# Kernel tuning notes

Hardware: AMD Instinct MI355X
Metric: run time of the kernel (lower is better)

The kernel has to match this reference:

```python
import jax, jax.numpy as jnp
import numpy as np

NEG = -1e9  # safe stand-in for log(0) in the one-hot initial state distribution


def setup_inputs() -> dict:
    key = jax.random.key(0)
    k1, k2 = jax.random.split(key)
    Q, S = 128, 96
    B, T = 2048, 48
    # log-space transition weights A[q, s, q']
    A = jax.random.normal(k1, (Q, S, Q), dtype=jnp.float32)
    # batch of symbol sequences
    xs = jax.random.randint(k2, (B, T), 0, S, dtype=jnp.int64)
    return {"A": A, "xs": xs}


def reference(A, xs):
    """FSA phonotactics log-likelihood: HMM-style forward algorithm in the log semiring.

    A:  [Q, S, Q] log-space weights (normalized per source state so that
        sum over (S, Q') of exp(A[q]) == 1, as in A_and_final_normalized).
    xs: [B, T] int symbol ids.
    Returns per-sequence log-likelihood [B] (final weights are all-ones).
    """
    Q, S, _ = A.shape
    B, T = xs.shape
    # normalize: each source state's outgoing mass sums to 1 in exp-space
    logZ = jax.nn.logsumexp(A.reshape(Q, -1), axis=-1)      # [Q]
    A_norm = A - logZ[:, None, None]                         # [Q, S, Q]
    # init = one-hot on state 0 (log-space)
    log_alpha0 = jnp.full((B, Q), NEG, dtype=A.dtype).at[:, 0].set(0.0)

    def step(log_alpha, tok):
        # tok: [B]; gather per-symbol transition matrices: [Q, B, Q]
        M = A_norm[:, tok, :]
        # alpha'[b, q'] = logsumexp_q( alpha[b, q] + M[q, b, q'] )
        la = jax.nn.logsumexp(log_alpha.T[:, :, None] + M, axis=0)  # [B, Q]
        return la, None

    log_alpha, _ = jax.lax.scan(step, log_alpha0, xs.T)  # scan over time
    # final = all ones -> vv(alpha, final) = sum over states (logsumexp in log space)
    return jax.nn.logsumexp(log_alpha, axis=-1)  # [B]
```

## Files before the change

kernel.cpp:

```cpp
#include <hip/hip_runtime.h>

#define QN 128
#define SN 96
#define TN 48
#define ROWSTRIDE (SN * QN)
#define NSEG 6
#define SEGLEN (ROWSTRIDE / NSEG)
#define SHIFT 10.0f
#define LOG255 5.5412635451584258f

#define U8_BYTES ((size_t)SN * QN * QN)
#define PART_OFF (U8_BYTES)
#define RMAX_OFF (PART_OFF + (size_t)QN * NSEG * 4)
#define LSC_OFF  (RMAX_OFF + (size_t)QN * NSEG * 4)
#define WS_NEED  (LSC_OFF + 16)

__global__ __launch_bounds__(256)
void fsa_stats(const float* __restrict__ A, float* __restrict__ part,
               float* __restrict__ rowmax) {
    const int bid = blockIdx.x;
    const int q   = bid / NSEG;
    const int seg = bid % NSEG;
    const int tid = threadIdx.x;
    const float* base = A + (size_t)q * ROWSTRIDE + seg * SEGLEN + tid * 8;

    const float4 v0 = *reinterpret_cast<const float4*>(base);
    const float4 v1 = *reinterpret_cast<const float4*>(base + 4);
    float s = (__expf(v0.x - SHIFT) + __expf(v0.y - SHIFT)) +
              (__expf(v0.z - SHIFT) + __expf(v0.w - SHIFT)) +
              (__expf(v1.x - SHIFT) + __expf(v1.y - SHIFT)) +
              (__expf(v1.z - SHIFT) + __expf(v1.w - SHIFT));
    float m = fmaxf(fmaxf(fmaxf(v0.x, v0.y), fmaxf(v0.z, v0.w)),
                    fmaxf(fmaxf(v1.x, v1.y), fmaxf(v1.z, v1.w)));

    __shared__ float reds[256];
    __shared__ float redm[256];
    reds[tid] = s; redm[tid] = m;
    __syncthreads();
    #pragma unroll
    for (int o = 128; o > 0; o >>= 1) {
        if (tid < o) {
            reds[tid] += reds[tid + o];
            redm[tid] = fmaxf(redm[tid], redm[tid + o]);
        }
        __syncthreads();
    }
    if (tid == 0) { part[bid] = reds[0]; rowmax[bid] = redm[0]; }
}

__global__ __launch_bounds__(256)
void fsa_write_u8(const float* __restrict__ A, const float* __restrict__ part,
                  const float* __restrict__ rowmax, uint* __restrict__ U,
                  float* __restrict__ logsc_p) {
    const int bid = blockIdx.x;
    const int kq  = bid / NSEG;
    const int seg = bid % NSEG;
    const int tid = threadIdx.x;

    __shared__ float lz[QN];
    __shared__ float dl[QN];
    if (tid < QN) {
        float z = 0.0f, rm = -1e30f;
        #pragma unroll
        for (int j = 0; j < NSEG; ++j) {
            z  += part[tid * NSEG + j];
            rm  = fmaxf(rm, rowmax[tid * NSEG + j]);
        }
        const float l = SHIFT + __logf(z);
        lz[tid] = l;
        dl[tid] = rm - l;
    }
    __syncthreads();
    #pragma unroll
    for (int o = 64; o > 0; o >>= 1) {
        if (tid < o) dl[tid] = fmaxf(dl[tid], dl[tid + o]);
        __syncthreads();
    }
    const float glob = dl[0];
    if (bid == 0 && tid == 0) logsc_p[0] = glob - LOG255;

    const int li = seg * SEGLEN + tid * 8;
    const int s  = li >> 7;
    const int qp = li & 127;

    uint d0 = 0, d1 = 0, d2 = 0, d3 = 0, d4 = 0, d5 = 0, d6 = 0, d7 = 0;
    #pragma unroll
    for (int j = 0; j < 4; ++j) {
        const int k = 4 * kq + j;
        const float* src = A + (size_t)k * ROWSTRIDE + li;
        const float off = lz[k] + glob;
        const float4 v0 = *reinterpret_cast<const float4*>(src);
        const float4 v1 = *reinterpret_cast<const float4*>(src + 4);
        const int sh = 8 * j;
        d0 |= ((uint)(255.0f * __expf(v0.x - off) + 0.5f)) << sh;
        d1 |= ((uint)(255.0f * __expf(v0.y - off) + 0.5f)) << sh;
        d2 |= ((uint)(255.0f * __expf(v0.z - off) + 0.5f)) << sh;
        d3 |= ((uint)(255.0f * __expf(v0.w - off) + 0.5f)) << sh;
        d4 |= ((uint)(255.0f * __expf(v1.x - off) + 0.5f)) << sh;
        d5 |= ((uint)(255.0f * __expf(v1.y - off) + 0.5f)) << sh;
        d6 |= ((uint)(255.0f * __expf(v1.z - off) + 0.5f)) << sh;
        d7 |= ((uint)(255.0f * __expf(v1.w - off) + 0.5f)) << sh;
    }
    uint* dst = U + (size_t)s * (QN * QN / 4) + kq * QN + qp;
    *reinterpret_cast<uint4*>(dst)     = make_uint4(d0, d1, d2, d3);
    *reinterpret_cast<uint4*>(dst + 4) = make_uint4(d4, d5, d6, d7);
}

__global__ __launch_bounds__(256)
void fsa_forward_u8(const uint* __restrict__ U, const int* __restrict__ xs,
                    const float* __restrict__ logsc_p, float* __restrict__ out,
                    int B) {
    const int wv   = threadIdx.x >> 6;
    const int lane = threadIdx.x & 63;
    const int b    = blockIdx.x * 4 + wv;
    if (b >= B) return;

    __shared__ __align__(16) float sp[4][QN];
    __shared__ int stok[4][TN];

    if (lane < TN) stok[wv][lane] = xs[b * TN + lane];
    sp[wv][2 * lane]     = (lane == 0) ? 1.0f : 0.0f;
    sp[wv][2 * lane + 1] = 0.0f;
    const float logsc = logsc_p[0];
    float c = 0.0f;

    for (int t = 0; t < TN; ++t) {
        int tok = __builtin_amdgcn_readfirstlane(stok[wv][t]);
        tok = (tok < 0) ? 0 : ((tok >= SN) ? (SN - 1) : tok);
        const uint2* wp = reinterpret_cast<const uint2*>(
            U + (size_t)tok * (QN * QN / 4)) + lane;

        float a0 = 0.0f, a1 = 0.0f;
        #pragma unroll 8
        for (int kq = 0; kq < 32; ++kq) {
            const uint2 w   = wp[kq * 64];
            const float4 pv = *reinterpret_cast<const float4*>(&sp[wv][4 * kq]);
            a0 = fmaf(pv.x, (float)( w.x        & 0xffu), a0);
            a0 = fmaf(pv.y, (float)((w.x >>  8) & 0xffu), a0);
            a0 = fmaf(pv.z, (float)((w.x >> 16) & 0xffu), a0);
            a0 = fmaf(pv.w, (float)( w.x >> 24         ), a0);
            a1 = fmaf(pv.x, (float)( w.y        & 0xffu), a1);
            a1 = fmaf(pv.y, (float)((w.y >>  8) & 0xffu), a1);
            a1 = fmaf(pv.z, (float)((w.y >> 16) & 0xffu), a1);
            a1 = fmaf(pv.w, (float)( w.y >> 24         ), a1);
        }

        if ((t & 3) == 3) {
            float s2 = a0 + a1;
            #pragma unroll
            for (int off = 32; off > 0; off >>= 1) s2 += __shfl_xor(s2, off, 64);
            s2 = fmaxf(s2, 1e-30f);
            c += __logf(s2);
            const float inv = 1.0f / s2;
            a0 *= inv; a1 *= inv;
        }
        *reinterpret_cast<float2*>(&sp[wv][2 * lane]) = make_float2(a0, a1);
    }
    if (lane == 0) out[b] = c + (float)TN * logsc;
}


__global__ __launch_bounds__(256)
void fsa_normalize(float* __restrict__ A) {
    const int q   = blockIdx.x;
    const int tid = threadIdx.x;
    float* row = A + (size_t)q * ROWSTRIDE;
    __shared__ float red[256];
    float mx = -1e30f;
    for (int i = tid; i < ROWSTRIDE; i += 256) mx = fmaxf(mx, row[i]);
    red[tid] = mx;
    __syncthreads();
    #pragma unroll
    for (int s = 128; s > 0; s >>= 1) {
        if (tid < s) red[tid] = fmaxf(red[tid], red[tid + s]);
        __syncthreads();
    }
    const float bmax = red[0];
    __syncthreads();
    float sum = 0.0f;
    for (int i = tid; i < ROWSTRIDE; i += 256) sum += expf(row[i] - bmax);
    red[tid] = sum;
    __syncthreads();
    #pragma unroll
    for (int s = 128; s > 0; s >>= 1) {
        if (tid < s) red[tid] += red[tid + s];
        __syncthreads();
    }
    const float logZ = bmax + logf(red[0]);
    for (int i = tid; i < ROWSTRIDE; i += 256) row[i] = expf(row[i] - logZ);
}

__global__ __launch_bounds__(128)
void fsa_forward(const float* __restrict__ W, const int* __restrict__ xs,
                 float* __restrict__ out) {
    const int b = blockIdx.x;
    const int q = threadIdx.x;
    __shared__ __align__(16) float sp[QN];
    __shared__ float red[QN];
    __shared__ int  stok[TN];
    if (q < TN) stok[q] = xs[b * TN + q];
    sp[q] = (q == 0) ? 1.0f : 0.0f;
    float c = 0.0f;
    __syncthreads();
    for (int t = 0; t < TN; ++t) {
        const int tok = stok[t];
        const float* wp = W + ((size_t)tok << 7) + q;
        float a0 = 0.f, a1 = 0.f, a2 = 0.f, a3 = 0.f;
        #pragma unroll 8
        for (int k = 0; k < QN; k += 4) {
            const float4 pv = *reinterpret_cast<const float4*>(&sp[k]);
            a0 = fmaf(pv.x, wp[0 * ROWSTRIDE], a0);
            a1 = fmaf(pv.y, wp[1 * ROWSTRIDE], a1);
            a2 = fmaf(pv.z, wp[2 * ROWSTRIDE], a2);
            a3 = fmaf(pv.w, wp[3 * ROWSTRIDE], a3);
            wp += 4 * ROWSTRIDE;
        }
        float acc = (a0 + a1) + (a2 + a3);
        __syncthreads();
        if ((t & 7) == 7) {
            red[q] = acc;
            __syncthreads();
            #pragma unroll
            for (int s = 64; s > 0; s >>= 1) {
                if (q < s) red[q] += red[q + s];
                __syncthreads();
            }
            const float m = red[0];
            c += logf(m);
            sp[q] = acc * (1.0f / m);
            __syncthreads();
        } else {
            sp[q] = acc;
            __syncthreads();
        }
    }
    if (q == 0) out[b] = c;
}


extern "C" void kernel_launch(void* const* d_in, const int* in_sizes, int n_in,
                              void* d_out, int out_size, void* d_ws, size_t ws_size,
                              hipStream_t stream) {
    float* A      = (float*)d_in[0];
    const int* xs = (const int*)d_in[1];
    float* out    = (float*)d_out;
    const int B   = in_sizes[1] / TN;

    if (ws_size >= WS_NEED) {
        unsigned char* ws = (unsigned char*)d_ws;
        uint*  U8      = (uint*)ws;
        float* part    = (float*)(ws + PART_OFF);
        float* rowmax  = (float*)(ws + RMAX_OFF);
        float* logsc_p = (float*)(ws + LSC_OFF);
        hipLaunchKernelGGL(fsa_stats, dim3(QN * NSEG), dim3(256), 0, stream,
                           A, part, rowmax);
        hipLaunchKernelGGL(fsa_write_u8, dim3((QN / 4) * NSEG), dim3(256), 0, stream,
                           A, part, rowmax, U8, logsc_p);
        hipLaunchKernelGGL(fsa_forward_u8, dim3((B + 3) / 4), dim3(256), 0, stream,
                           U8, xs, logsc_p, out, B);
        return;
    }
    hipLaunchKernelGGL(fsa_normalize, dim3(QN), dim3(256), 0, stream, A);
    hipLaunchKernelGGL(fsa_forward, dim3(B), dim3(QN), 0, stream, A, xs, out);
}
```

Measured before the change: 162.2 us.

## Split each sequence across two wavefronts and use hardware ubyte conversion

The forward kernel now runs one sequence per 128-thread block, one output state per thread, instead of one sequence per wavefront with two states per lane. State vectors are double-buffered in shared memory and the normalization sum is combined across the two wavefronts through shared memory. The cross-lane shuffle reduction is therefore replaced by block-wide barriers every timestep. Byte unpacking uses the AMD cvt_f32_ubyte builtins instead of shift-and-mask, which cuts ALU work. Per-step latency should drop from the extra parallelism, at the cost of twice as many waves and a __syncthreads per step.

New measurement: 178.7 us. 1.1x slower.

```diff
diff --git a/kernel.cpp b/kernel.cpp
--- a/kernel.cpp
+++ b/kernel.cpp
@@ -14,6 +14,18 @@
 #define RMAX_OFF (PART_OFF + (size_t)QN * NSEG * 4)
 #define LSC_OFF  (RMAX_OFF + (size_t)QN * NSEG * 4)
 #define WS_NEED  (LSC_OFF + 16)
+
+#if __has_builtin(__builtin_amdgcn_cvt_f32_ubyte0)
+#define CVT_UB0(w) __builtin_amdgcn_cvt_f32_ubyte0(w)
+#define CVT_UB1(w) __builtin_amdgcn_cvt_f32_ubyte1(w)
+#define CVT_UB2(w) __builtin_amdgcn_cvt_f32_ubyte2(w)
+#define CVT_UB3(w) __builtin_amdgcn_cvt_f32_ubyte3(w)
+#else
+#define CVT_UB0(w) ((float)((w) & 0xffu))
+#define CVT_UB1(w) ((float)(((w) >> 8) & 0xffu))
+#define CVT_UB2(w) ((float)(((w) >> 16) & 0xffu))
+#define CVT_UB3(w) ((float)((w) >> 24))
+#endif
 
 __global__ __launch_bounds__(256)
 void fsa_stats(const float* __restrict__ A, float* __restrict__ part,
@@ -106,57 +118,58 @@
     *reinterpret_cast<uint4*>(dst + 4) = make_uint4(d4, d5, d6, d7);
 }
 
-__global__ __launch_bounds__(256)
-void fsa_forward_u8(const uint* __restrict__ U, const int* __restrict__ xs,
-                    const float* __restrict__ logsc_p, float* __restrict__ out,
-                    int B) {
-    const int wv   = threadIdx.x >> 6;
-    const int lane = threadIdx.x & 63;
-    const int b    = blockIdx.x * 4 + wv;
+__global__ __launch_bounds__(128)
+void fsa_forward_u8s(const uint* __restrict__ U, const int* __restrict__ xs,
+                     const float* __restrict__ logsc_p, float* __restrict__ out,
+                     int B) {
+    const int tid = threadIdx.x;
+    const int b   = blockIdx.x;
     if (b >= B) return;
 
-    __shared__ __align__(16) float sp[4][QN];
-    __shared__ int stok[4][TN];
-
-    if (lane < TN) stok[wv][lane] = xs[b * TN + lane];
-    sp[wv][2 * lane]     = (lane == 0) ? 1.0f : 0.0f;
-    sp[wv][2 * lane + 1] = 0.0f;
+    __shared__ __align__(16) float sp[2][QN];
+    __shared__ int   stok[TN];
+    __shared__ float wsum[2];
+
+    if (tid < TN) stok[tid] = xs[b * TN + tid];
+    sp[0][tid] = (tid == 0) ? 1.0f : 0.0f;
     const float logsc = logsc_p[0];
     float c = 0.0f;
-
+    __syncthreads();
+
+    int cur = 0;
     for (int t = 0; t < TN; ++t) {
-        int tok = __builtin_amdgcn_readfirstlane(stok[wv][t]);
+        int tok = __builtin_amdgcn_readfirstlane(stok[t]);
         tok = (tok < 0) ? 0 : ((tok >= SN) ? (SN - 1) : tok);
-        const uint2* wp = reinterpret_cast<const uint2*>(
-            U + (size_t)tok * (QN * QN / 4)) + lane;
-
-        float a0 = 0.0f, a1 = 0.0f;
+        const uint* wp = U + (size_t)tok * (QN * QN / 4) + tid;
+        const float* p = sp[cur];
+
+        float a0 = 0.0f, a1 = 0.0f, a2 = 0.0f, a3 = 0.0f;
         #pragma unroll 8
         for (int kq = 0; kq < 32; ++kq) {
-            const uint2 w   = wp[kq * 64];
-            const float4 pv = *reinterpret_cast<const float4*>(&sp[wv][4 * kq]);
-            a0 = fmaf(pv.x, (float)( w.x        & 0xffu), a0);
-            a0 = fmaf(pv.y, (float)((w.x >>  8) & 0xffu), a0);
-            a0 = fmaf(pv.z, (float)((w.x >> 16) & 0xffu), a0);
-            a0 = fmaf(pv.w, (float)( w.x >> 24         ), a0);
-            a1 = fmaf(pv.x, (float)( w.y        & 0xffu), a1);
-            a1 = fmaf(pv.y, (float)((w.y >>  8) & 0xffu), a1);
-            a1 = fmaf(pv.z, (float)((w.y >> 16) & 0xffu), a1);
-            a1 = fmaf(pv.w, (float)( w.y >> 24         ), a1);
-        }
+            const uint  w  = wp[kq * QN];
+            const float4 pv = *reinterpret_cast<const float4*>(&p[4 * kq]);
+            a0 = fmaf(pv.x, CVT_UB0(w), a0);
+            a1 = fmaf(pv.y, CVT_UB1(w), a1);
+            a2 = fmaf(pv.z, CVT_UB2(w), a2);
+            a3 = fmaf(pv.w, CVT_UB3(w), a3);
+        }
+        float a = (a0 + a1) + (a2 + a3);
 
         if ((t & 3) == 3) {
-            float s2 = a0 + a1;
+            float s = a;
             #pragma unroll
-            for (int off = 32; off > 0; off >>= 1) s2 += __shfl_xor(s2, off, 64);
-            s2 = fmaxf(s2, 1e-30f);
-            c += __logf(s2);
-            const float inv = 1.0f / s2;
-            a0 *= inv; a1 *= inv;
-        }
-        *reinterpret_cast<float2*>(&sp[wv][2 * lane]) = make_float2(a0, a1);
-    }
-    if (lane == 0) out[b] = c + (float)TN * logsc;
+            for (int off = 32; off > 0; off >>= 1) s += __shfl_xor(s, off, 64);
+            if ((tid & 63) == 0) wsum[tid >> 6] = s;
+            __syncthreads();
+            const float tot = fmaxf(wsum[0] + wsum[1], 1e-30f);
+            c += __logf(tot);
+            a *= (1.0f / tot);
+        }
+        sp[cur ^ 1][tid] = a;
+        cur ^= 1;
+        __syncthreads();
+    }
+    if (tid == 0) out[b] = c + (float)TN * logsc;
 }
 
 
@@ -256,7 +269,7 @@
                            A, part, rowmax);
         hipLaunchKernelGGL(fsa_write_u8, dim3((QN / 4) * NSEG), dim3(256), 0, stream,
                            A, part, rowmax, U8, logsc_p);
-        hipLaunchKernelGGL(fsa_forward_u8, dim3((B + 3) / 4), dim3(256), 0, stream,
+        hipLaunchKernelGGL(fsa_forward_u8s, dim3(B), dim3(128), 0, stream,
                            U8, xs, logsc_p, out, B);
         return;
     }
```

## Double-buffer next timestep's u8 transition slice in registers during forward recursion

Applied to the files above, without the earlier changes.

The forward kernel now prefetches the next token's 128x128 u8 transition slice into a second register buffer while the current step computes, so global/L2 load latency overlaps the FMA chain. It also uses the hardware ubyte-to-float conversion builtins instead of shift/mask/convert, and splits each accumulator into two to shorten FMA dependency chains. The launch bounds now request two blocks per SIMD group. Holding 64 extra VGPRs of buffered data raises register pressure and may cut occupancy or cause spills.

Measured after the change: 183.8 us. +13.3%, slower.

```diff
diff --git a/kernel.cpp b/kernel.cpp
--- a/kernel.cpp
+++ b/kernel.cpp
@@ -14,6 +14,18 @@
 #define RMAX_OFF (PART_OFF + (size_t)QN * NSEG * 4)
 #define LSC_OFF  (RMAX_OFF + (size_t)QN * NSEG * 4)
 #define WS_NEED  (LSC_OFF + 16)
+
+#if __has_builtin(__builtin_amdgcn_cvt_f32_ubyte0)
+#define CVT_UB0(w) __builtin_amdgcn_cvt_f32_ubyte0(w)
+#define CVT_UB1(w) __builtin_amdgcn_cvt_f32_ubyte1(w)
+#define CVT_UB2(w) __builtin_amdgcn_cvt_f32_ubyte2(w)
+#define CVT_UB3(w) __builtin_amdgcn_cvt_f32_ubyte3(w)
+#else
+#define CVT_UB0(w) ((float)((w) & 0xffu))
+#define CVT_UB1(w) ((float)(((w) >> 8) & 0xffu))
+#define CVT_UB2(w) ((float)(((w) >> 16) & 0xffu))
+#define CVT_UB3(w) ((float)((w) >> 24))
+#endif
 
 __global__ __launch_bounds__(256)
 void fsa_stats(const float* __restrict__ A, float* __restrict__ part,
@@ -106,10 +118,10 @@
     *reinterpret_cast<uint4*>(dst + 4) = make_uint4(d4, d5, d6, d7);
 }
 
-__global__ __launch_bounds__(256)
-void fsa_forward_u8(const uint* __restrict__ U, const int* __restrict__ xs,
-                    const float* __restrict__ logsc_p, float* __restrict__ out,
-                    int B) {
+__global__ __launch_bounds__(256, 2)
+void fsa_forward_u8p(const uint* __restrict__ U, const int* __restrict__ xs,
+                     const float* __restrict__ logsc_p, float* __restrict__ out,
+                     int B) {
     const int wv   = threadIdx.x >> 6;
     const int lane = threadIdx.x & 63;
     const int b    = blockIdx.x * 4 + wv;
@@ -124,38 +136,77 @@
     const float logsc = logsc_p[0];
     float c = 0.0f;
 
-    for (int t = 0; t < TN; ++t) {
-        int tok = __builtin_amdgcn_readfirstlane(stok[wv][t]);
-        tok = (tok < 0) ? 0 : ((tok >= SN) ? (SN - 1) : tok);
-        const uint2* wp = reinterpret_cast<const uint2*>(
-            U + (size_t)tok * (QN * QN / 4)) + lane;
-
-        float a0 = 0.0f, a1 = 0.0f;
-        #pragma unroll 8
-        for (int kq = 0; kq < 32; ++kq) {
-            const uint2 w   = wp[kq * 64];
-            const float4 pv = *reinterpret_cast<const float4*>(&sp[wv][4 * kq]);
-            a0 = fmaf(pv.x, (float)( w.x        & 0xffu), a0);
-            a0 = fmaf(pv.y, (float)((w.x >>  8) & 0xffu), a0);
-            a0 = fmaf(pv.z, (float)((w.x >> 16) & 0xffu), a0);
-            a0 = fmaf(pv.w, (float)( w.x >> 24         ), a0);
-            a1 = fmaf(pv.x, (float)( w.y        & 0xffu), a1);
-            a1 = fmaf(pv.y, (float)((w.y >>  8) & 0xffu), a1);
-            a1 = fmaf(pv.z, (float)((w.y >> 16) & 0xffu), a1);
-            a1 = fmaf(pv.w, (float)( w.y >> 24         ), a1);
-        }
-
-        if ((t & 3) == 3) {
-            float s2 = a0 + a1;
-            #pragma unroll
-            for (int off = 32; off > 0; off >>= 1) s2 += __shfl_xor(s2, off, 64);
-            s2 = fmaxf(s2, 1e-30f);
-            c += __logf(s2);
-            const float inv = 1.0f / s2;
-            a0 *= inv; a1 *= inv;
-        }
-        *reinterpret_cast<float2*>(&sp[wv][2 * lane]) = make_float2(a0, a1);
-    }
+    uint2 bufA[32], bufB[32];
+
+#define SLICE_PTR(T, WPVAR)                                                    \
+    {                                                                          \
+        int tok_ = __builtin_amdgcn_readfirstlane(stok[wv][(T)]);              \
+        tok_ = (tok_ < 0) ? 0 : ((tok_ >= SN) ? (SN - 1) : tok_);              \
+        WPVAR = reinterpret_cast<const uint2*>(                                \
+                    U + (size_t)tok_ * (QN * QN / 4)) + lane;                  \
+    }
+
+#define LOADBUF(BUF, WP)                                                       \
+    {                                                                          \
+        _Pragma("unroll")                                                      \
+        for (int i_ = 0; i_ < 32; ++i_) BUF[i_] = WP[i_ * 64];                 \
+    }
+
+#define COMPUTE(BUF, R0, R1)                                                   \
+    float R0, R1;                                                              \
+    {                                                                          \
+        float a0 = 0.f, a0b = 0.f, a1 = 0.f, a1b = 0.f;                        \
+        _Pragma("unroll")                                                      \
+        for (int i_ = 0; i_ < 32; ++i_) {                                      \
+            const float4 pv =                                                  \
+                *reinterpret_cast<const float4*>(&sp[wv][4 * i_]);             \
+            const uint wx = BUF[i_].x, wy = BUF[i_].y;                         \
+            a0  = fmaf(pv.x, CVT_UB0(wx), a0);                                 \
+            a0b = fmaf(pv.y, CVT_UB1(wx), a0b);                                \
+            a0  = fmaf(pv.z, CVT_UB2(wx), a0);                                 \
+            a0b = fmaf(pv.w, CVT_UB3(wx), a0b);                                \
+            a1  = fmaf(pv.x, CVT_UB0(wy), a1);                                 \
+            a1b = fmaf(pv.y, CVT_UB1(wy), a1b);                                \
+            a1  = fmaf(pv.z, CVT_UB2(wy), a1);                                 \
+            a1b = fmaf(pv.w, CVT_UB3(wy), a1b);                                \
+        }                                                                      \
+        R0 = a0 + a0b; R1 = a1 + a1b;                                          \
+    }
+
+    {
+        const uint2* wp; SLICE_PTR(0, wp); LOADBUF(bufA, wp);
+    }
+
+    #pragma unroll 1
+    for (int t = 0; t < TN; t += 2) {
+        {
+            const uint2* wp; SLICE_PTR(t + 1, wp); LOADBUF(bufB, wp);
+        }
+        {
+            COMPUTE(bufA, r0, r1);
+            *reinterpret_cast<float2*>(&sp[wv][2 * lane]) = make_float2(r0, r1);
+        }
+        if (t + 2 < TN) {
+            const uint2* wp; SLICE_PTR(t + 2, wp); LOADBUF(bufA, wp);
+        }
+        {
+            COMPUTE(bufB, r0, r1);
+            if (((t + 1) & 3) == 3) {
+                float s = r0 + r1;
+                #pragma unroll
+                for (int off = 32; off > 0; off >>= 1)
+                    s += __shfl_xor(s, off, 64);
+                s = fmaxf(s, 1e-30f);
+                c += __logf(s);
+                const float inv = 1.0f / s;
+                r0 *= inv; r1 *= inv;
+            }
+            *reinterpret_cast<float2*>(&sp[wv][2 * lane]) = make_float2(r0, r1);
+        }
+    }
+#undef SLICE_PTR
+#undef LOADBUF
+#undef COMPUTE
     if (lane == 0) out[b] = c + (float)TN * logsc;
 }
 
@@ -256,7 +307,7 @@
                            A, part, rowmax);
         hipLaunchKernelGGL(fsa_write_u8, dim3((QN / 4) * NSEG), dim3(256), 0, stream,
                            A, part, rowmax, U8, logsc_p);
-        hipLaunchKernelGGL(fsa_forward_u8, dim3((B + 3) / 4), dim3(256), 0, stream,
+        hipLaunchKernelGGL(fsa_forward_u8p, dim3((B + 3) / 4), dim3(256), 0, stream,
                            U8, xs, logsc_p, out, B);
         return;
     }
```
